# Optimization experiments

Hardware: AMD Instinct MI355X
Metric: run time of the kernel (lower is better)

The kernel has to match this reference:

```python
import jax, jax.numpy as jnp
import numpy as np

P = 64       # number of pathways
NV = 512     # features per pathway (nvar[i])
W = 256      # hidden width per pathway
COV = 16     # covariates
B = 2048     # batch
EPS = 1e-5   # BatchNorm eps
SLOPE = 0.2  # LeakyReLU negative slope


def _lrelu(v):
    return jnp.where(v >= 0, v, SLOPE * v)


def setup_inputs() -> dict:
    key = jax.random.key(0)
    ks = jax.random.split(key, 8)
    x = jax.random.normal(ks[0], (B, P * NV + COV), dtype=jnp.float32)
    # per-pathway weights (no bias), stacked across pathways -> grouped GEMM
    W1 = jax.random.normal(ks[1], (P, NV, W), dtype=jnp.float32) * (1.0 / np.sqrt(NV))
    W2 = jax.random.normal(ks[2], (P, W, W), dtype=jnp.float32) * (1.0 / np.sqrt(W))
    W3 = jax.random.normal(ks[3], (P, W), dtype=jnp.float32) * (1.0 / np.sqrt(W))
    gamma = jnp.ones((P,), dtype=jnp.float32)   # bn_path weight
    beta = jnp.zeros((P,), dtype=jnp.float32)   # bn_path bias
    fc_w = jax.random.normal(ks[4], (P + COV, 1), dtype=jnp.float32) * 0.05
    fc_b = jnp.full((1,), 0.001, dtype=jnp.float32)
    return {"x": x, "W1": W1, "W2": W2, "W3": W3,
            "gamma": gamma, "beta": beta, "fc_w": fc_w, "fc_b": fc_b}


def reference(x, W1, W2, W3, gamma, beta, fc_w, fc_b):
    # pathway blocks (dropout = identity in eval): grouped GEMMs over P pathways
    xp = x[:, : P * NV].reshape(B, P, NV)
    h = _lrelu(jnp.einsum('bpi,pio->bpo', xp, W1))
    h = _lrelu(jnp.einsum('bpi,pio->bpo', h, W2))
    p = _lrelu(jnp.einsum('bpi,pi->bp', h, W3))          # [B, P]
    # BatchNorm1d (training-mode batch statistics, biased variance)
    mean = p.mean(axis=0)
    var = p.var(axis=0)
    pn = (p - mean) / jnp.sqrt(var + EPS) * gamma + beta
    # global L2 (Frobenius) normalization, as torch.norm(pathway_layer, 2)
    pn = pn / jnp.linalg.norm(pn)
    # concat covariates, final linear + sigmoid
    z = jnp.concatenate([pn, x[:, P * NV: P * NV + COV]], axis=1)  # [B, P+COV]
    return jax.nn.sigmoid(z @ fc_w + fc_b)                         # [B, 1]
```

## Files before the change

kernel.cpp:

```cpp
#include <hip/hip_runtime.h>
#include <hip/hip_bf16.h>

#define PW 64
#define NV 512
#define HW 256
#define COV 16
#define BATCH 2048
#define XROW (PW * NV + COV)

typedef short s16x8 __attribute__((ext_vector_type(8)));
typedef float f32x4 __attribute__((ext_vector_type(4)));

__device__ __forceinline__ unsigned short f2bf(float f) {
    union { float f; unsigned int u; } v;
    v.f = f;
    unsigned int u = v.u;
    unsigned int r = (u + 0x7fffu + ((u >> 16) & 1u)) >> 16;
    return (unsigned short)r;
}

__device__ __forceinline__ float bf2f(unsigned short h) {
    union { unsigned int u; float f; } v;
    v.u = ((unsigned int)h) << 16;
    return v.f;
}

__global__ __launch_bounds__(256)
void transpose_convert(const float* __restrict__ in, unsigned short* __restrict__ out,
                       int R, int C) {
    __shared__ float tile[32][33];
    const int p = blockIdx.z;
    const int c0 = blockIdx.x * 32;
    const int r0 = blockIdx.y * 32;
    const float* ip = in + (size_t)p * R * C;
    unsigned short* op = out + (size_t)p * R * C;
    const int tx = threadIdx.x;
    const int ty = threadIdx.y;
    #pragma unroll
    for (int j = 0; j < 32; j += 8)
        tile[ty + j][tx] = ip[(size_t)(r0 + ty + j) * C + c0 + tx];
    __syncthreads();
    #pragma unroll
    for (int j = 0; j < 32; j += 8)
        op[(size_t)(c0 + ty + j) * R + r0 + tx] = f2bf(tile[tx][ty + j]);
}

template<int K, bool CONV_A>
__global__ __launch_bounds__(256)
void gemm_lrelu(const void* __restrict__ Abase, const unsigned short* __restrict__ BT,
                unsigned short* __restrict__ Cout,
                int lda, long aPs, long bPs, long cPs) {
    __shared__ __align__(16) unsigned short As[128][72];
    __shared__ __align__(16) unsigned short Bs[128][72];

    const int p   = blockIdx.z;
    const int bm0 = blockIdx.x * 128;
    const int bn0 = blockIdx.y * 128;
    const int t    = threadIdx.x;
    const int lane = t & 63;
    const int wave = t >> 6;
    const int wm = (wave >> 1) * 64;
    const int wn = (wave & 1) * 64;
    const int l15  = lane & 15;
    const int quad = lane >> 4;

    f32x4 acc[4][4] = {};

    const unsigned short* Bp = BT + (size_t)p * bPs;

    for (int k0 = 0; k0 < K; k0 += 64) {
        if (CONV_A) {
            const float* Ap = (const float*)Abase + (size_t)p * aPs;
            #pragma unroll
            for (int i = 0; i < 8; ++i) {
                int idx = t + i * 256;
                int row = idx >> 4;
                int c4  = (idx & 15) * 4;
                float4 v = *(const float4*)(Ap + (size_t)(bm0 + row) * lda + k0 + c4);
                ushort4 u;
                u.x = f2bf(v.x); u.y = f2bf(v.y); u.z = f2bf(v.z); u.w = f2bf(v.w);
                *(ushort4*)&As[row][c4] = u;
            }
        } else {
            const unsigned short* Ap = (const unsigned short*)Abase + (size_t)p * aPs;
            #pragma unroll
            for (int i = 0; i < 4; ++i) {
                int idx = t + i * 256;
                int row = idx >> 3;
                int c8  = (idx & 7) * 8;
                *(s16x8*)&As[row][c8] = *(const s16x8*)(Ap + (size_t)(bm0 + row) * lda + k0 + c8);
            }
        }
        #pragma unroll
        for (int i = 0; i < 4; ++i) {
            int idx = t + i * 256;
            int row = idx >> 3;
            int c8  = (idx & 7) * 8;
            *(s16x8*)&Bs[row][c8] = *(const s16x8*)(Bp + (size_t)(bn0 + row) * K + k0 + c8);
        }
        __syncthreads();

        #pragma unroll
        for (int kk = 0; kk < 64; kk += 32) {
            s16x8 af[4], bfr[4];
            #pragma unroll
            for (int mi = 0; mi < 4; ++mi)
                af[mi] = *(const s16x8*)&As[wm + mi * 16 + l15][kk + quad * 8];
            #pragma unroll
            for (int ni = 0; ni < 4; ++ni)
                bfr[ni] = *(const s16x8*)&Bs[wn + ni * 16 + l15][kk + quad * 8];
            #pragma unroll
            for (int mi = 0; mi < 4; ++mi)
                #pragma unroll
                for (int ni = 0; ni < 4; ++ni)
                    acc[mi][ni] = __builtin_amdgcn_mfma_f32_16x16x32_bf16(
                        af[mi], bfr[ni], acc[mi][ni], 0, 0, 0);
        }
        __syncthreads();
    }

    unsigned short* Cp = Cout + (size_t)p * cPs;
    #pragma unroll
    for (int mi = 0; mi < 4; ++mi) {
        #pragma unroll
        for (int ni = 0; ni < 4; ++ni) {
            int col = bn0 + wn + ni * 16 + l15;
            #pragma unroll
            for (int r = 0; r < 4; ++r) {
                int row = bm0 + wm + mi * 16 + quad * 4 + r;
                float v = acc[mi][ni][r];
                v = v >= 0.f ? v : 0.2f * v;
                Cp[(size_t)row * HW + col] = f2bf(v);
            }
        }
    }
}

__global__ __launch_bounds__(256)
void pathdot(const unsigned short* __restrict__ H2, const float* __restrict__ W3,
             float* __restrict__ pvec) {
    const int p    = blockIdx.y;
    const int wave = threadIdx.x >> 6;
    const int lane = threadIdx.x & 63;
    const int b    = blockIdx.x * 4 + wave;
    const unsigned short* h = H2 + ((size_t)p * BATCH + b) * HW + lane * 4;
    const float* w = W3 + (size_t)p * HW + lane * 4;
    ushort4 hv = *(const ushort4*)h;
    float4  wv = *(const float4*)w;
    float s = bf2f(hv.x) * wv.x + bf2f(hv.y) * wv.y +
              bf2f(hv.z) * wv.z + bf2f(hv.w) * wv.w;
    #pragma unroll
    for (int off = 32; off; off >>= 1) s += __shfl_down(s, off);
    if (lane == 0) {
        float v = s >= 0.f ? s : 0.2f * s;
        pvec[(size_t)p * BATCH + b] = v;
    }
}

__global__ __launch_bounds__(256)
void stats1(const float* __restrict__ pvec, float* __restrict__ sums) {
    const int p = blockIdx.x;
    float s = 0.f, q = 0.f;
    for (int i = threadIdx.x; i < BATCH; i += 256) {
        float v = pvec[(size_t)p * BATCH + i];
        s += v; q += v * v;
    }
    #pragma unroll
    for (int off = 32; off; off >>= 1) {
        s += __shfl_down(s, off);
        q += __shfl_down(q, off);
    }
    __shared__ float ls[4], lq[4];
    const int wave = threadIdx.x >> 6, lane = threadIdx.x & 63;
    if (lane == 0) { ls[wave] = s; lq[wave] = q; }
    __syncthreads();
    if (threadIdx.x == 0) {
        sums[p]      = ls[0] + ls[1] + ls[2] + ls[3];
        sums[64 + p] = lq[0] + lq[1] + lq[2] + lq[3];
    }
}

__global__ void stats2(const float* __restrict__ sums, const float* __restrict__ gamma,
                       const float* __restrict__ beta, float* __restrict__ stat) {
    const int p = threadIdx.x;
    float S = sums[p], Q = sums[64 + p];
    float mean = S * (1.f / BATCH);
    float var  = Q * (1.f / BATCH) - mean * mean;
    float invstd = rsqrtf(var + 1e-5f);
    stat[p]      = mean;
    stat[64 + p] = invstd;
    float g = gamma[p], bt = beta[p];
    float contrib = (float)BATCH * (g * g * var / (var + 1e-5f) + bt * bt);
    #pragma unroll
    for (int off = 32; off; off >>= 1) contrib += __shfl_down(contrib, off);
    if (p == 0) stat[128] = rsqrtf(contrib);
}

__global__ __launch_bounds__(256)
void final_k(const float* __restrict__ pvec, const float* __restrict__ stat,
             const float* __restrict__ gamma, const float* __restrict__ beta,
             const float* __restrict__ x, const float* __restrict__ fc_w,
             const float* __restrict__ fc_b, float* __restrict__ out) {
    const int b = blockIdx.x * 256 + threadIdx.x;
    const float rn = stat[128];
    float acc = fc_b[0];
    #pragma unroll
    for (int p = 0; p < PW; ++p) {
        float pn = (pvec[(size_t)p * BATCH + b] - stat[p]) * stat[64 + p] * gamma[p] + beta[p];
        acc += pn * rn * fc_w[p];
    }
    #pragma unroll
    for (int c = 0; c < COV; ++c)
        acc += x[(size_t)b * XROW + PW * NV + c] * fc_w[PW + c];
    out[b] = 1.f / (1.f + __expf(-acc));
}

extern "C" void kernel_launch(void* const* d_in, const int* in_sizes, int n_in,
                              void* d_out, int out_size, void* d_ws, size_t ws_size,
                              hipStream_t stream) {
    const float* x     = (const float*)d_in[0];
    const float* W1    = (const float*)d_in[1];
    const float* W2    = (const float*)d_in[2];
    const float* W3    = (const float*)d_in[3];
    const float* gamma = (const float*)d_in[4];
    const float* beta  = (const float*)d_in[5];
    const float* fc_w  = (const float*)d_in[6];
    const float* fc_b  = (const float*)d_in[7];
    float* out = (float*)d_out;

    char* ws = (char*)d_ws;
    size_t off = 0;
    unsigned short* W1T = (unsigned short*)(ws + off); off += (size_t)PW * NV * HW * 2;
    unsigned short* W2T = (unsigned short*)(ws + off); off += (size_t)PW * HW * HW * 2;
    unsigned short* H1  = (unsigned short*)(ws + off); off += (size_t)PW * BATCH * HW * 2;
    unsigned short* H2  = (unsigned short*)(ws + off); off += (size_t)PW * BATCH * HW * 2;
    float* pvec = (float*)(ws + off); off += (size_t)PW * BATCH * 4;
    float* sums = (float*)(ws + off); off += 256 * 4;
    float* stat = (float*)(ws + off); off += 256 * 4;

    transpose_convert<<<dim3(HW / 32, NV / 32, PW), dim3(32, 8), 0, stream>>>(W1, W1T, NV, HW);
    transpose_convert<<<dim3(HW / 32, HW / 32, PW), dim3(32, 8), 0, stream>>>(W2, W2T, HW, HW);

    gemm_lrelu<NV, true><<<dim3(BATCH / 128, HW / 128, PW), 256, 0, stream>>>(
        (const void*)x, W1T, H1, XROW, (long)NV, (long)HW * NV, (long)BATCH * HW);

    gemm_lrelu<HW, false><<<dim3(BATCH / 128, HW / 128, PW), 256, 0, stream>>>(
        (const void*)H1, W2T, H2, HW, (long)BATCH * HW, (long)HW * HW, (long)BATCH * HW);

    pathdot<<<dim3(BATCH / 4, PW), 256, 0, stream>>>(H2, W3, pvec);

    stats1<<<PW, 256, 0, stream>>>(pvec, sums);
    stats2<<<1, 64, 0, stream>>>(sums, gamma, beta, stat);

    final_k<<<BATCH / 256, 256, 0, stream>>>(pvec, stat, gamma, beta, x, fc_w, fc_b, out);
}
```

Baseline: 515.8 us.

## Widen GEMM tile to full hidden width and fuse W3 dot into second GEMM

Each GEMM block now covers all 256 output columns (128x256 tile, 4x8 MFMA accumulators per wave). The second layer's epilogue does the LeakyReLU, the dot with W3 and a cross-lane and shared-memory reduction, then writes pvec directly. This drops the H2 buffer and the separate pathdot kernel, and layer 1 reads each A tile only once. In exchange it uses more registers and shared memory per block, and launches half as many blocks (1024 per GEMM), which may lower occupancy.

```diff
diff --git a/kernel.cpp b/kernel.cpp
--- a/kernel.cpp
+++ b/kernel.cpp
@@ -45,28 +45,29 @@
         op[(size_t)(c0 + ty + j) * R + r0 + tx] = f2bf(tile[tx][ty + j]);
 }
 
-template<int K, bool CONV_A>
-__global__ __launch_bounds__(256)
-void gemm_lrelu(const void* __restrict__ Abase, const unsigned short* __restrict__ BT,
-                unsigned short* __restrict__ Cout,
-                int lda, long aPs, long bPs, long cPs) {
+template<int K, bool CONV_A, bool FUSE>
+__global__ __launch_bounds__(256)
+void gemm_fused(const void* __restrict__ Abase, const unsigned short* __restrict__ BT,
+                unsigned short* __restrict__ Hout, const float* __restrict__ W3,
+                float* __restrict__ pvec, int lda, long aPs) {
     __shared__ __align__(16) unsigned short As[128][72];
-    __shared__ __align__(16) unsigned short Bs[128][72];
+    __shared__ __align__(16) unsigned short Bs[256][72];
+    __shared__ float red[2][128];
 
     const int p   = blockIdx.z;
     const int bm0 = blockIdx.x * 128;
-    const int bn0 = blockIdx.y * 128;
     const int t    = threadIdx.x;
     const int lane = t & 63;
     const int wave = t >> 6;
-    const int wm = (wave >> 1) * 64;
-    const int wn = (wave & 1) * 64;
+    const int wm  = (wave & 1) * 64;
+    const int wni = wave >> 1;
+    const int wn  = wni * 128;
     const int l15  = lane & 15;
     const int quad = lane >> 4;
 
-    f32x4 acc[4][4] = {};
-
-    const unsigned short* Bp = BT + (size_t)p * bPs;
+    f32x4 acc[4][8] = {};
+
+    const unsigned short* Bp = BT + (size_t)p * HW * K;
 
     for (int k0 = 0; k0 < K; k0 += 64) {
         if (CONV_A) {
@@ -92,68 +93,89 @@
             }
         }
         #pragma unroll
-        for (int i = 0; i < 4; ++i) {
+        for (int i = 0; i < 8; ++i) {
             int idx = t + i * 256;
             int row = idx >> 3;
             int c8  = (idx & 7) * 8;
-            *(s16x8*)&Bs[row][c8] = *(const s16x8*)(Bp + (size_t)(bn0 + row) * K + k0 + c8);
+            *(s16x8*)&Bs[row][c8] = *(const s16x8*)(Bp + (size_t)row * K + k0 + c8);
         }
         __syncthreads();
 
         #pragma unroll
         for (int kk = 0; kk < 64; kk += 32) {
-            s16x8 af[4], bfr[4];
+            s16x8 af[4], bfr[8];
             #pragma unroll
             for (int mi = 0; mi < 4; ++mi)
                 af[mi] = *(const s16x8*)&As[wm + mi * 16 + l15][kk + quad * 8];
             #pragma unroll
-            for (int ni = 0; ni < 4; ++ni)
+            for (int ni = 0; ni < 8; ++ni)
                 bfr[ni] = *(const s16x8*)&Bs[wn + ni * 16 + l15][kk + quad * 8];
             #pragma unroll
             for (int mi = 0; mi < 4; ++mi)
                 #pragma unroll
-                for (int ni = 0; ni < 4; ++ni)
+                for (int ni = 0; ni < 8; ++ni)
                     acc[mi][ni] = __builtin_amdgcn_mfma_f32_16x16x32_bf16(
                         af[mi], bfr[ni], acc[mi][ni], 0, 0, 0);
         }
         __syncthreads();
     }
 
-    unsigned short* Cp = Cout + (size_t)p * cPs;
-    #pragma unroll
-    for (int mi = 0; mi < 4; ++mi) {
-        #pragma unroll
-        for (int ni = 0; ni < 4; ++ni) {
-            int col = bn0 + wn + ni * 16 + l15;
+    if (!FUSE) {
+        unsigned short* Cp = Hout + (size_t)p * BATCH * HW;
+        #pragma unroll
+        for (int mi = 0; mi < 4; ++mi) {
+            #pragma unroll
+            for (int ni = 0; ni < 8; ++ni) {
+                int col = wn + ni * 16 + l15;
+                #pragma unroll
+                for (int r = 0; r < 4; ++r) {
+                    int row = bm0 + wm + mi * 16 + quad * 4 + r;
+                    float v = acc[mi][ni][r];
+                    v = v >= 0.f ? v : 0.2f * v;
+                    Cp[(size_t)row * HW + col] = f2bf(v);
+                }
+            }
+        }
+    } else {
+        float w3v[8];
+        #pragma unroll
+        for (int ni = 0; ni < 8; ++ni)
+            w3v[ni] = W3[(size_t)p * HW + wn + ni * 16 + l15];
+        float part[4][4];
+        #pragma unroll
+        for (int mi = 0; mi < 4; ++mi) {
             #pragma unroll
             for (int r = 0; r < 4; ++r) {
-                int row = bm0 + wm + mi * 16 + quad * 4 + r;
-                float v = acc[mi][ni][r];
-                v = v >= 0.f ? v : 0.2f * v;
-                Cp[(size_t)row * HW + col] = f2bf(v);
-            }
-        }
-    }
-}
-
-__global__ __launch_bounds__(256)
-void pathdot(const unsigned short* __restrict__ H2, const float* __restrict__ W3,
-             float* __restrict__ pvec) {
-    const int p    = blockIdx.y;
-    const int wave = threadIdx.x >> 6;
-    const int lane = threadIdx.x & 63;
-    const int b    = blockIdx.x * 4 + wave;
-    const unsigned short* h = H2 + ((size_t)p * BATCH + b) * HW + lane * 4;
-    const float* w = W3 + (size_t)p * HW + lane * 4;
-    ushort4 hv = *(const ushort4*)h;
-    float4  wv = *(const float4*)w;
-    float s = bf2f(hv.x) * wv.x + bf2f(hv.y) * wv.y +
-              bf2f(hv.z) * wv.z + bf2f(hv.w) * wv.w;
-    #pragma unroll
-    for (int off = 32; off; off >>= 1) s += __shfl_down(s, off);
-    if (lane == 0) {
-        float v = s >= 0.f ? s : 0.2f * s;
-        pvec[(size_t)p * BATCH + b] = v;
+                float s = 0.f;
+                #pragma unroll
+                for (int ni = 0; ni < 8; ++ni) {
+                    float v = acc[mi][ni][r];
+                    v = v >= 0.f ? v : 0.2f * v;
+                    s += v * w3v[ni];
+                }
+                part[mi][r] = s;
+            }
+        }
+        #pragma unroll
+        for (int off = 1; off < 16; off <<= 1)
+            #pragma unroll
+            for (int mi = 0; mi < 4; ++mi)
+                #pragma unroll
+                for (int r = 0; r < 4; ++r)
+                    part[mi][r] += __shfl_xor(part[mi][r], off);
+        if (l15 == 0) {
+            #pragma unroll
+            for (int mi = 0; mi < 4; ++mi)
+                #pragma unroll
+                for (int r = 0; r < 4; ++r)
+                    red[wni][wm + mi * 16 + quad * 4 + r] = part[mi][r];
+        }
+        __syncthreads();
+        if (t < 128) {
+            float s = red[0][t] + red[1][t];
+            s = s >= 0.f ? s : 0.2f * s;
+            pvec[(size_t)p * BATCH + bm0 + t] = s;
+        }
     }
 }
 
@@ -233,7 +255,6 @@
     unsigned short* W1T = (unsigned short*)(ws + off); off += (size_t)PW * NV * HW * 2;
     unsigned short* W2T = (unsigned short*)(ws + off); off += (size_t)PW * HW * HW * 2;
     unsigned short* H1  = (unsigned short*)(ws + off); off += (size_t)PW * BATCH * HW * 2;
-    unsigned short* H2  = (unsigned short*)(ws + off); off += (size_t)PW * BATCH * HW * 2;
     float* pvec = (float*)(ws + off); off += (size_t)PW * BATCH * 4;
     float* sums = (float*)(ws + off); off += 256 * 4;
     float* stat = (float*)(ws + off); off += 256 * 4;
@@ -241,13 +262,11 @@
     transpose_convert<<<dim3(HW / 32, NV / 32, PW), dim3(32, 8), 0, stream>>>(W1, W1T, NV, HW);
     transpose_convert<<<dim3(HW / 32, HW / 32, PW), dim3(32, 8), 0, stream>>>(W2, W2T, HW, HW);
 
-    gemm_lrelu<NV, true><<<dim3(BATCH / 128, HW / 128, PW), 256, 0, stream>>>(
-        (const void*)x, W1T, H1, XROW, (long)NV, (long)HW * NV, (long)BATCH * HW);
-
-    gemm_lrelu<HW, false><<<dim3(BATCH / 128, HW / 128, PW), 256, 0, stream>>>(
-        (const void*)H1, W2T, H2, HW, (long)BATCH * HW, (long)HW * HW, (long)BATCH * HW);
-
-    pathdot<<<dim3(BATCH / 4, PW), 256, 0, stream>>>(H2, W3, pvec);
+    gemm_fused<NV, true, false><<<dim3(BATCH / 128, 1, PW), 256, 0, stream>>>(
+        (const void*)x, W1T, H1, nullptr, nullptr, XROW, (long)NV);
+
+    gemm_fused<HW, false, true><<<dim3(BATCH / 128, 1, PW), 256, 0, stream>>>(
+        (const void*)H1, W2T, nullptr, W3, pvec, HW, (long)BATCH * HW);
 
     stats1<<<PW, 256, 0, stream>>>(pvec, sums);
     stats2<<<1, 64, 0, stream>>>(sums, gamma, beta, stat);
```

Result: no change. 517.6 us (+0.4%).
